# Performance work log

Hardware: AMD Instinct MI355X
Metric: run time of the kernel (lower is better)

## Reference

```python
import jax, jax.numpy as jnp
import numpy as np

EPS = 1e-5  # torch nn.LayerNorm default

def _ln(x, g, b):
    # LayerNorm over last dim with per-position affine params g, b (broadcastable)
    m = jnp.mean(x, axis=-1, keepdims=True)
    v = jnp.mean((x - m) ** 2, axis=-1, keepdims=True)
    return (x - m) * jax.lax.rsqrt(v + EPS) * g + b

def _mlp_ln(s, W1, b1, W2, b2, g, b):
    # Linear -> SiLU -> Linear -> LayerNorm
    h = jax.nn.silu(s @ W1 + b1) @ W2 + b2
    return _ln(h, g, b)

def setup_inputs() -> dict:
    key = jax.random.key(0)
    B, S, D = 4, 2048, 1024
    MEM, NOI, RES = 512, 64, 32
    ks = jax.random.split(key, 40)
    ki = iter(range(40))
    def nrm(shape, scale=0.02):
        return (jax.random.normal(ks[next(ki)], shape, jnp.float32) * scale)
    def gamma(shape):
        return jnp.ones(shape, jnp.float32) + nrm(shape)
    inp = {
        'x': jax.random.normal(ks[next(ki)], (B, S, D), jnp.float32),
        'pathway_ids': jax.random.randint(ks[next(ki)], (B, S), 0, 1000),
        'compartment_ids': jax.random.randint(ks[next(ki)], (B, S), 0, 5),
        'time_steps': jax.random.randint(ks[next(ki)], (B, S), 0, 5),
        'scale_type': jax.random.randint(ks[next(ki)], (B, S), 0, 3),
        'memory_state': jax.random.normal(ks[next(ki)], (B, MEM), jnp.float32),
        'noise_state': jax.random.normal(ks[next(ki)], (B, NOI), jnp.float32),
        'resource_state': jax.random.normal(ks[next(ki)], (B, RES), jnp.float32),
        # per-pathway / compartment / time / scale LayerNorm affine tables
        'pw_g': gamma((1000, D)), 'pw_b': nrm((1000, D)),
        'cp_g': gamma((5, D)), 'cp_b': nrm((5, D)),
        'tm_g': gamma((5, D)), 'tm_b': nrm((5, D)),
        'ms_g': gamma((3, D)), 'ms_b': nrm((3, D)),
        # memory / stochastic / resource MLP+LN stacks
        'mem_W1': nrm((MEM, D)), 'mem_b1': jnp.zeros((D,)), 'mem_W2': nrm((D, D)), 'mem_b2': jnp.zeros((D,)), 'mem_g': gamma((D,)), 'mem_be': jnp.zeros((D,)),
        'noi_W1': nrm((NOI, D)), 'noi_b1': jnp.zeros((D,)), 'noi_W2': nrm((D, D)), 'noi_b2': jnp.zeros((D,)), 'noi_g': gamma((D,)), 'noi_be': jnp.zeros((D,)),
        'res_W1': nrm((RES, D)), 'res_b1': jnp.zeros((D,)), 'res_W2': nrm((D, D)), 'res_b2': jnp.zeros((D,)), 'res_g': gamma((D,)), 'res_be': jnp.zeros((D,)),
        # integration MLP+LN
        'int_W1': nrm((6 * D, D)), 'int_b1': jnp.zeros((D,)), 'int_W2': nrm((D, D)), 'int_b2': jnp.zeros((D,)), 'int_g': gamma((D,)), 'int_be': jnp.zeros((D,)),
        'aw': jnp.ones((6,), jnp.float32) / 6.0,
    }
    return inp

def reference(x, pathway_ids, compartment_ids, time_steps, scale_type,
              memory_state, noise_state, resource_state,
              pw_g, pw_b, cp_g, cp_b, tm_g, tm_b, ms_g, ms_b,
              mem_W1, mem_b1, mem_W2, mem_b2, mem_g, mem_be,
              noi_W1, noi_b1, noi_W2, noi_b2, noi_g, noi_be,
              res_W1, res_b1, res_W2, res_b2, res_g, res_be,
              int_W1, int_b1, int_W2, int_b2, int_g, int_be, aw):
    # hierarchical: pathway-indexed LN, then compartment-indexed LN on its output
    h = _ln(x, pw_g[pathway_ids], pw_b[pathway_ids])
    h = _ln(h, cp_g[compartment_ids], cp_b[compartment_ids])
    # temporal: time-step-indexed LN of x
    t = _ln(x, tm_g[time_steps], tm_b[time_steps])
    # state-conditioned additive effects, broadcast over seq
    m = x + _mlp_ln(memory_state, mem_W1, mem_b1, mem_W2, mem_b2, mem_g, mem_be)[:, None, :]
    n = x + _mlp_ln(noise_state, noi_W1, noi_b1, noi_W2, noi_b2, noi_g, noi_be)[:, None, :]
    r = x + _mlp_ln(resource_state, res_W1, res_b1, res_W2, res_b2, res_g, res_be)[:, None, :]
    # multiscale: scale-indexed LN (scale in {0,1,2})
    s = _ln(x, ms_g[scale_type], ms_b[scale_type])
    w = jax.nn.softmax(aw)
    cat = jnp.concatenate([w[0] * h, w[1] * t, w[2] * m, w[3] * n, w[4] * r, w[5] * s], axis=-1)
    return _mlp_ln(cat, int_W1, int_b1, int_W2, int_b2, int_g, int_be)
```

## Files before the change

kernel.cpp:

```cpp
#include <hip/hip_runtime.h>
#include <cstdint>
#include <cstddef>

#define EPS_LN 1e-5f

typedef short bf16x8 __attribute__((ext_vector_type(8)));
typedef float f32x4 __attribute__((ext_vector_type(4)));
typedef unsigned int u32_gl __attribute__((address_space(1)));
typedef unsigned int u32_ld __attribute__((address_space(3)));

__device__ __forceinline__ unsigned short f2bf(float f) {
  union { float f; unsigned u; } v; v.f = f;
  unsigned r = v.u + 0x7fffu + ((v.u >> 16) & 1u);
  return (unsigned short)(r >> 16);
}

__device__ __forceinline__ float block_sum256(float v, float* red) {
  for (int m = 32; m > 0; m >>= 1) v += __shfl_xor(v, m, 64);
  const int lane = threadIdx.x & 63, w = threadIdx.x >> 6;
  if (lane == 0) red[w] = v;
  __syncthreads();
  float r = red[0] + red[1] + red[2] + red[3];
  __syncthreads();
  return r;
}

__global__ __launch_bounds__(256) void setup_small(
    const float* __restrict__ aw,
    const float* __restrict__ mb1, const float* __restrict__ nb1, const float* __restrict__ rb1,
    const float* __restrict__ mb2, const float* __restrict__ nb2, const float* __restrict__ rb2,
    const float* __restrict__ ib1,
    float* __restrict__ w, float* __restrict__ H1pre, float* __restrict__ Ys,
    float* __restrict__ bias1) {
  const int bi = blockIdx.x;
  if (bi == 0) {
    if (threadIdx.x == 0) {
      float m = aw[0];
      for (int i = 1; i < 6; ++i) m = fmaxf(m, aw[i]);
      float e[6], s = 0.f;
      for (int i = 0; i < 6; ++i) { e[i] = __expf(aw[i] - m); s += e[i]; }
      for (int i = 0; i < 6; ++i) w[i] = e[i] / s;
    }
    return;
  }
  if (bi <= 48) {
    const int idx = (bi - 1) * 256 + threadIdx.x;
    const int st = idx >> 12;
    const float* b1 = st == 0 ? mb1 : st == 1 ? nb1 : rb1;
    H1pre[idx] = b1[idx & 1023];
    return;
  }
  if (bi <= 96) {
    const int idx = (bi - 49) * 256 + threadIdx.x;
    const int st = idx >> 12;
    const float* b2 = st == 0 ? mb2 : st == 1 ? nb2 : rb2;
    Ys[idx] = b2[idx & 1023];
    return;
  }
  const int idx = (bi - 97) * 256 + threadIdx.x;
  bias1[idx] = ib1[idx & 1023];
}

__global__ __launch_bounds__(256) void state_h1_acc(
    const float* __restrict__ mem, const float* __restrict__ noi, const float* __restrict__ res,
    const float* __restrict__ mW1, const float* __restrict__ nW1, const float* __restrict__ rW1,
    float* __restrict__ H1pre) {
  const int chunk = blockIdx.x, ks = blockIdx.y;
  const int j = chunk * 128 + (threadIdx.x & 127);
  const int half = threadIdx.x >> 7;
  int st, k0, klen, sstride;
  const float* W1; const float* sp;
  if (ks < 8)       { st = 0; W1 = mW1; sp = mem; sstride = 512; k0 = ks * 64 + half * 32; klen = 32; }
  else if (ks == 8) { st = 1; W1 = nW1; sp = noi; sstride = 64;  k0 = half * 32;           klen = 32; }
  else              { st = 2; W1 = rW1; sp = res; sstride = 32;  k0 = half * 16;           klen = 16; }
  float a0 = 0.f, a1 = 0.f, a2 = 0.f, a3 = 0.f;
  const float* wp = W1 + (size_t)k0 * 1024 + j;
  for (int it = 0; it < klen; ++it) {
    const float wv = wp[(size_t)it * 1024];
    const int k = k0 + it;
    a0 += sp[k] * wv;
    a1 += sp[sstride + k] * wv;
    a2 += sp[2 * sstride + k] * wv;
    a3 += sp[3 * sstride + k] * wv;
  }
  __shared__ float part[4][128];
  const int jl = threadIdx.x & 127;
  if (half) { part[0][jl] = a0; part[1][jl] = a1; part[2][jl] = a2; part[3][jl] = a3; }
  __syncthreads();
  if (!half) {
    atomicAdd(&H1pre[(size_t)(st * 4 + 0) * 1024 + j], a0 + part[0][jl]);
    atomicAdd(&H1pre[(size_t)(st * 4 + 1) * 1024 + j], a1 + part[1][jl]);
    atomicAdd(&H1pre[(size_t)(st * 4 + 2) * 1024 + j], a2 + part[2][jl]);
    atomicAdd(&H1pre[(size_t)(st * 4 + 3) * 1024 + j], a3 + part[3][jl]);
  }
}

__global__ __launch_bounds__(256) void state_y_acc(
    const float* __restrict__ H1pre,
    const float* __restrict__ mW2, const float* __restrict__ nW2, const float* __restrict__ rW2,
    float* __restrict__ Ys) {
  const int chunk = blockIdx.x, ks = blockIdx.y, st = blockIdx.z;
  const float* W2 = st == 0 ? mW2 : st == 1 ? nW2 : rW2;
  const int j = chunk * 128 + (threadIdx.x & 127);
  const int half = threadIdx.x >> 7;
  const int k0 = ks * 64 + half * 32;
  const float* h1 = H1pre + (size_t)st * 4096;
  float a0 = 0.f, a1 = 0.f, a2 = 0.f, a3 = 0.f;
  const float* wp = W2 + (size_t)k0 * 1024 + j;
  for (int it = 0; it < 32; ++it) {
    const float wv = wp[(size_t)it * 1024];
    const int k = k0 + it;
    float h;
    h = h1[k];        a0 += (h / (1.f + __expf(-h))) * wv;
    h = h1[1024 + k]; a1 += (h / (1.f + __expf(-h))) * wv;
    h = h1[2048 + k]; a2 += (h / (1.f + __expf(-h))) * wv;
    h = h1[3072 + k]; a3 += (h / (1.f + __expf(-h))) * wv;
  }
  __shared__ float part[4][128];
  const int jl = threadIdx.x & 127;
  if (half) { part[0][jl] = a0; part[1][jl] = a1; part[2][jl] = a2; part[3][jl] = a3; }
  __syncthreads();
  if (!half) {
    atomicAdd(&Ys[(size_t)(st * 4 + 0) * 1024 + j], a0 + part[0][jl]);
    atomicAdd(&Ys[(size_t)(st * 4 + 1) * 1024 + j], a1 + part[1][jl]);
    atomicAdd(&Ys[(size_t)(st * 4 + 2) * 1024 + j], a2 + part[2][jl]);
    atomicAdd(&Ys[(size_t)(st * 4 + 3) * 1024 + j], a3 + part[3][jl]);
  }
}

__global__ __launch_bounds__(256) void state_ln(
    const float* __restrict__ Ys,
    const float* __restrict__ mg, const float* __restrict__ mbe,
    const float* __restrict__ ng, const float* __restrict__ nbe,
    const float* __restrict__ rg, const float* __restrict__ rbe,
    const float* __restrict__ w, float* __restrict__ mnrv) {
  __shared__ float red[4];
  const int st = blockIdx.x >> 2, b = blockIdx.x & 3;
  const float* g  = st == 0 ? mg  : st == 1 ? ng  : rg;
  const float* be = st == 0 ? mbe : st == 1 ? nbe : rbe;
  const float* y = Ys + (size_t)blockIdx.x * 1024;
  const int j = threadIdx.x * 4;
  float4 yv4 = *(const float4*)(y + j);
  float yv[4] = { yv4.x, yv4.y, yv4.z, yv4.w };
  float s = yv[0] + yv[1] + yv[2] + yv[3];
  float ss = yv[0]*yv[0] + yv[1]*yv[1] + yv[2]*yv[2] + yv[3]*yv[3];
  s = block_sum256(s, red);
  ss = block_sum256(ss, red);
  const float mu = s * (1.f / 1024.f);
  const float rstd = rsqrtf(ss * (1.f / 1024.f) - mu * mu + EPS_LN);
  float4 g4 = *(const float4*)(g + j);
  float4 b4 = *(const float4*)(be + j);
  const float sc = w[2 + st];
  float* out = mnrv + (size_t)b * 3072 + st * 1024;
  out[j]     = ((yv[0] - mu) * rstd * g4.x + b4.x) * sc;
  out[j + 1] = ((yv[1] - mu) * rstd * g4.y + b4.y) * sc;
  out[j + 2] = ((yv[2] - mu) * rstd * g4.z + b4.z) * sc;
  out[j + 3] = ((yv[3] - mu) * rstd * g4.w + b4.w) * sc;
}

__global__ __launch_bounds__(256) void bias1_kernel(
    const float* __restrict__ mnrv, const float* __restrict__ iW1,
    float* __restrict__ bias1) {
  const int chunk = blockIdx.x, ks = blockIdx.y;
  const int j = chunk * 128 + (threadIdx.x & 127);
  const int half = threadIdx.x >> 7;
  const int g0 = ks * 64 + half * 32;
  float acc0 = 0.f, acc1 = 0.f, acc2 = 0.f, acc3 = 0.f;
  const float* wp = iW1 + (size_t)(2048 + g0) * 1024 + j;
  for (int it = 0; it < 32; ++it) {
    const int g = g0 + it;
    const float wv = wp[(size_t)it * 1024];
    acc0 += mnrv[g] * wv;
    acc1 += mnrv[3072 + g] * wv;
    acc2 += mnrv[6144 + g] * wv;
    acc3 += mnrv[9216 + g] * wv;
  }
  __shared__ float part[4][128];
  const int jl = threadIdx.x & 127;
  if (half) { part[0][jl] = acc0; part[1][jl] = acc1; part[2][jl] = acc2; part[3][jl] = acc3; }
  __syncthreads();
  if (!half) {
    atomicAdd(&bias1[j],        acc0 + part[0][jl]);
    atomicAdd(&bias1[1024 + j], acc1 + part[1][jl]);
    atomicAdd(&bias1[2048 + j], acc2 + part[2][jl]);
    atomicAdd(&bias1[3072 + j], acc3 + part[3][jl]);
  }
}

__global__ __launch_bounds__(256) void build_w1t(
    const float* __restrict__ W1, const float* __restrict__ w,
    unsigned short* __restrict__ W1T) {
  __shared__ float tile[32][33];
  const int k0 = blockIdx.x * 32, n0 = blockIdx.y * 32;
  const int r = threadIdx.x >> 3;
  const int c = (threadIdx.x & 7) * 4;
  const int kk = k0 + r;
  float v[4];
  if (kk < 2048) {
    const float s = (kk < 1024) ? w[0] : w[1];
    float4 a = *(const float4*)(W1 + (size_t)kk * 1024 + n0 + c);
    v[0] = s * a.x; v[1] = s * a.y; v[2] = s * a.z; v[3] = s * a.w;
  } else if (kk < 3072) {
    const float s2 = w[2], s3 = w[3], s4 = w[4];
    float4 a = *(const float4*)(W1 + (size_t)kk * 1024 + n0 + c);
    float4 bq = *(const float4*)(W1 + (size_t)(kk + 1024) * 1024 + n0 + c);
    float4 cq = *(const float4*)(W1 + (size_t)(kk + 2048) * 1024 + n0 + c);
    v[0] = s2 * a.x + s3 * bq.x + s4 * cq.x;
    v[1] = s2 * a.y + s3 * bq.y + s4 * cq.y;
    v[2] = s2 * a.z + s3 * bq.z + s4 * cq.z;
    v[3] = s2 * a.w + s3 * bq.w + s4 * cq.w;
  } else {
    const float s = w[5];
    float4 a = *(const float4*)(W1 + (size_t)(kk + 2048) * 1024 + n0 + c);
    v[0] = s * a.x; v[1] = s * a.y; v[2] = s * a.z; v[3] = s * a.w;
  }
  tile[r][c] = v[0]; tile[r][c + 1] = v[1]; tile[r][c + 2] = v[2]; tile[r][c + 3] = v[3];
  __syncthreads();
  const int nl = threadIdx.x >> 3;
  const int k4 = (threadIdx.x & 7) * 4;
  ushort4 o;
  o.x = f2bf(tile[k4][nl]);     o.y = f2bf(tile[k4 + 1][nl]);
  o.z = f2bf(tile[k4 + 2][nl]); o.w = f2bf(tile[k4 + 3][nl]);
  *(ushort4*)(W1T + (size_t)(n0 + nl) * 4096 + k0 + k4) = o;
}

__global__ __launch_bounds__(256) void build_w2t(
    const float* __restrict__ W2, unsigned short* __restrict__ W2T) {
  __shared__ float tile[32][33];
  const int k0 = blockIdx.x * 32, n0 = blockIdx.y * 32;
  const int r = threadIdx.x >> 3, c = (threadIdx.x & 7) * 4;
  float4 a = *(const float4*)(W2 + (size_t)(k0 + r) * 1024 + n0 + c);
  tile[r][c] = a.x; tile[r][c + 1] = a.y; tile[r][c + 2] = a.z; tile[r][c + 3] = a.w;
  __syncthreads();
  const int nl = threadIdx.x >> 3, k4 = (threadIdx.x & 7) * 4;
  ushort4 o;
  o.x = f2bf(tile[k4][nl]);     o.y = f2bf(tile[k4 + 1][nl]);
  o.z = f2bf(tile[k4 + 2][nl]); o.w = f2bf(tile[k4 + 3][nl]);
  *(ushort4*)(W2T + (size_t)(n0 + nl) * 1024 + k0 + k4) = o;
}

__global__ __launch_bounds__(256) void build_cat(
    const float* __restrict__ x,
    const int* __restrict__ pid_, const int* __restrict__ cid_,
    const int* __restrict__ tid_, const int* __restrict__ sid_,
    const float* __restrict__ pwg, const float* __restrict__ pwb,
    const float* __restrict__ cpg, const float* __restrict__ cpb,
    const float* __restrict__ tmg, const float* __restrict__ tmb,
    const float* __restrict__ msg, const float* __restrict__ msb,
    unsigned short* __restrict__ cat4) {
  __shared__ float red[4];
  const int row = blockIdx.x;
  const int j = threadIdx.x * 4;
  float4 xv4 = *(const float4*)(x + (size_t)row * 1024 + j);
  float xv[4] = { xv4.x, xv4.y, xv4.z, xv4.w };
  float s = xv[0] + xv[1] + xv[2] + xv[3];
  float ss = xv[0]*xv[0] + xv[1]*xv[1] + xv[2]*xv[2] + xv[3]*xv[3];
  s = block_sum256(s, red);
  ss = block_sum256(ss, red);
  const float mu = s * (1.f / 1024.f);
  const float rstd = rsqrtf(ss * (1.f / 1024.f) - mu * mu + EPS_LN);
  float xh[4];
  for (int q = 0; q < 4; ++q) xh[q] = (xv[q] - mu) * rstd;
  const int pid = pid_[row], cid = cid_[row], tmi = tid_[row], msi = sid_[row];
  unsigned short* crow = cat4 + (size_t)row * 4096;

  float4 g4 = *(const float4*)(pwg + (size_t)pid * 1024 + j);
  float4 b4 = *(const float4*)(pwb + (size_t)pid * 1024 + j);
  float h1[4];
  h1[0] = xh[0] * g4.x + b4.x; h1[1] = xh[1] * g4.y + b4.y;
  h1[2] = xh[2] * g4.z + b4.z; h1[3] = xh[3] * g4.w + b4.w;
  float s1 = h1[0] + h1[1] + h1[2] + h1[3];
  float ss1 = h1[0]*h1[0] + h1[1]*h1[1] + h1[2]*h1[2] + h1[3]*h1[3];
  s1 = block_sum256(s1, red);
  ss1 = block_sum256(ss1, red);
  const float mu1 = s1 * (1.f / 1024.f);
  const float rstd1 = rsqrtf(ss1 * (1.f / 1024.f) - mu1 * mu1 + EPS_LN);
  g4 = *(const float4*)(cpg + (size_t)cid * 1024 + j);
  b4 = *(const float4*)(cpb + (size_t)cid * 1024 + j);
  ushort4 o;
  o.x = f2bf((h1[0] - mu1) * rstd1 * g4.x + b4.x);
  o.y = f2bf((h1[1] - mu1) * rstd1 * g4.y + b4.y);
  o.z = f2bf((h1[2] - mu1) * rstd1 * g4.z + b4.z);
  o.w = f2bf((h1[3] - mu1) * rstd1 * g4.w + b4.w);
  *(ushort4*)(crow + j) = o;

  g4 = *(const float4*)(tmg + (size_t)tmi * 1024 + j);
  b4 = *(const float4*)(tmb + (size_t)tmi * 1024 + j);
  o.x = f2bf(xh[0] * g4.x + b4.x); o.y = f2bf(xh[1] * g4.y + b4.y);
  o.z = f2bf(xh[2] * g4.z + b4.z); o.w = f2bf(xh[3] * g4.w + b4.w);
  *(ushort4*)(crow + 1024 + j) = o;

  o.x = f2bf(xv[0]); o.y = f2bf(xv[1]); o.z = f2bf(xv[2]); o.w = f2bf(xv[3]);
  *(ushort4*)(crow + 2048 + j) = o;

  g4 = *(const float4*)(msg + (size_t)msi * 1024 + j);
  b4 = *(const float4*)(msb + (size_t)msi * 1024 + j);
  o.x = f2bf(xh[0] * g4.x + b4.x); o.y = f2bf(xh[1] * g4.y + b4.y);
  o.z = f2bf(xh[2] * g4.z + b4.z); o.w = f2bf(xh[3] * g4.w + b4.w);
  *(ushort4*)(crow + 3072 + j) = o;
}

template <int EPI>
__global__ __launch_bounds__(128, 4) void gemm_bt(
    const unsigned short* __restrict__ A, const unsigned short* __restrict__ BT,
    const float* __restrict__ bias, void* __restrict__ out, int K) {
  __shared__ unsigned short At[64 * 32];
  __shared__ unsigned short Bt[128 * 32];
  const int t = threadIdx.x;
  const int lane = t & 63;
  const int wc = t >> 6;
  const int quad = lane >> 4, l16 = lane & 15;
  const int bm = blockIdx.x, bn = blockIdx.y;
  const unsigned short* Ab = A + (size_t)bm * 64 * K;
  const unsigned short* Bb = BT + (size_t)bn * 128 * K;
  const int r0 = t >> 2, c0 = (t & 3) * 8;
  f32x4 acc[4][4];
#pragma unroll
  for (int i = 0; i < 4; ++i)
#pragma unroll
    for (int jj = 0; jj < 4; ++jj) { f32x4 z = {0.f, 0.f, 0.f, 0.f}; acc[i][jj] = z; }

  for (int kt = 0; kt < K; kt += 32) {
    __builtin_amdgcn_global_load_lds(
        (const u32_gl*)(Ab + (size_t)r0 * K + kt + c0),
        (u32_ld*)(At + t * 8), 16, 0, 0);
    __builtin_amdgcn_global_load_lds(
        (const u32_gl*)(Ab + (size_t)(r0 + 32) * K + kt + c0),
        (u32_ld*)(At + (128 + t) * 8), 16, 0, 0);
    __builtin_amdgcn_global_load_lds(
        (const u32_gl*)(Bb + (size_t)r0 * K + kt + c0),
        (u32_ld*)(Bt + t * 8), 16, 0, 0);
    __builtin_amdgcn_global_load_lds(
        (const u32_gl*)(Bb + (size_t)(r0 + 32) * K + kt + c0),
        (u32_ld*)(Bt + (128 + t) * 8), 16, 0, 0);
    __builtin_amdgcn_global_load_lds(
        (const u32_gl*)(Bb + (size_t)(r0 + 64) * K + kt + c0),
        (u32_ld*)(Bt + (256 + t) * 8), 16, 0, 0);
    __builtin_amdgcn_global_load_lds(
        (const u32_gl*)(Bb + (size_t)(r0 + 96) * K + kt + c0),
        (u32_ld*)(Bt + (384 + t) * 8), 16, 0, 0);
    __syncthreads();
    bf16x8 aF[4], bF[4];
#pragma unroll
    for (int mi = 0; mi < 4; ++mi)
      aF[mi] = *(const bf16x8*)(At + (mi * 16 + l16) * 32 + quad * 8);
#pragma unroll
    for (int ni = 0; ni < 4; ++ni)
      bF[ni] = *(const bf16x8*)(Bt + (wc * 64 + ni * 16 + l16) * 32 + quad * 8);
#pragma unroll
    for (int mi = 0; mi < 4; ++mi)
#pragma unroll
      for (int ni = 0; ni < 4; ++ni)
        acc[mi][ni] = __builtin_amdgcn_mfma_f32_16x16x32_bf16(aF[mi], bF[ni], acc[mi][ni], 0, 0, 0);
    __syncthreads();
  }
#pragma unroll
  for (int mi = 0; mi < 4; ++mi) {
#pragma unroll
    for (int ni = 0; ni < 4; ++ni) {
      const int col = bn * 128 + wc * 64 + ni * 16 + l16;
#pragma unroll
      for (int r = 0; r < 4; ++r) {
        const int row = bm * 64 + mi * 16 + quad * 4 + r;
        float v = acc[mi][ni][r];
        if (EPI == 1) {
          v += bias[(size_t)(row >> 11) * 1024 + col];
          v = v / (1.f + __expf(-v));
          ((unsigned short*)out)[(size_t)row * 1024 + col] = f2bf(v);
        } else {
          v += bias[col];
          ((float*)out)[(size_t)row * 1024 + col] = v;
        }
      }
    }
  }
}

__global__ __launch_bounds__(256) void final_ln(
    const float* __restrict__ Y, const float* __restrict__ g,
    const float* __restrict__ be, float* __restrict__ out) {
  __shared__ float red[4];
  const int row = blockIdx.x;
  const int j = threadIdx.x * 4;
  float4 yv4 = *(const float4*)(Y + (size_t)row * 1024 + j);
  float yv[4] = { yv4.x, yv4.y, yv4.z, yv4.w };
  float s = yv[0] + yv[1] + yv[2] + yv[3];
  float ss = yv[0]*yv[0] + yv[1]*yv[1] + yv[2]*yv[2] + yv[3]*yv[3];
  s = block_sum256(s, red);
  ss = block_sum256(ss, red);
  const float mu = s * (1.f / 1024.f);
  const float rstd = rsqrtf(ss * (1.f / 1024.f) - mu * mu + EPS_LN);
  float4 g4 = *(const float4*)(g + j);
  float4 b4 = *(const float4*)(be + j);
  float4 o;
  o.x = (yv[0] - mu) * rstd * g4.x + b4.x;
  o.y = (yv[1] - mu) * rstd * g4.y + b4.y;
  o.z = (yv[2] - mu) * rstd * g4.z + b4.z;
  o.w = (yv[3] - mu) * rstd * g4.w + b4.w;
  *(float4*)(out + (size_t)row * 1024 + j) = o;
}

extern "C" void kernel_launch(void* const* d_in, const int* in_sizes, int n_in,
                              void* d_out, int out_size, void* d_ws, size_t ws_size,
                              hipStream_t stream) {
  const float* x   = (const float*)d_in[0];
  const int*   pid = (const int*)d_in[1];
  const int*   cid = (const int*)d_in[2];
  const int*   tms = (const int*)d_in[3];
  const int*   sct = (const int*)d_in[4];
  const float* mem = (const float*)d_in[5];
  const float* noi = (const float*)d_in[6];
  const float* res = (const float*)d_in[7];
  const float* pwg = (const float*)d_in[8];
  const float* pwb = (const float*)d_in[9];
  const float* cpg = (const float*)d_in[10];
  const float* cpb = (const float*)d_in[11];
  const float* tmg = (const float*)d_in[12];
  const float* tmb = (const float*)d_in[13];
  const float* msg = (const float*)d_in[14];
  const float* msb = (const float*)d_in[15];
  const float* mW1 = (const float*)d_in[16]; const float* mb1 = (const float*)d_in[17];
  const float* mW2 = (const float*)d_in[18]; const float* mb2 = (const float*)d_in[19];
  const float* mg  = (const float*)d_in[20]; const float* mbe = (const float*)d_in[21];
  const float* nW1 = (const float*)d_in[22]; const float* nb1 = (const float*)d_in[23];
  const float* nW2 = (const float*)d_in[24]; const float* nb2 = (const float*)d_in[25];
  const float* ng  = (const float*)d_in[26]; const float* nbe = (const float*)d_in[27];
  const float* rW1 = (const float*)d_in[28]; const float* rb1 = (const float*)d_in[29];
  const float* rW2 = (const float*)d_in[30]; const float* rb2 = (const float*)d_in[31];
  const float* rg  = (const float*)d_in[32]; const float* rbe = (const float*)d_in[33];
  const float* iW1 = (const float*)d_in[34]; const float* ib1 = (const float*)d_in[35];
  const float* iW2 = (const float*)d_in[36]; const float* ib2 = (const float*)d_in[37];
  const float* ig  = (const float*)d_in[38]; const float* ibe = (const float*)d_in[39];
  const float* aw  = (const float*)d_in[40];

  char* ws = (char*)d_ws;
  float* w6    = (float*)ws;
  float* H1pre = w6 + 16;
  float* Ys    = H1pre + 12288;
  float* mnrv  = Ys + 12288;
  float* bias1 = mnrv + 12288;
  unsigned short* W1T  = (unsigned short*)(ws + (1ull << 20));
  unsigned short* W2T  = (unsigned short*)(ws + (9ull << 20));
  unsigned short* cat4 = (unsigned short*)(ws + (11ull << 20));
  unsigned short* Hb   = (unsigned short*)(ws + (75ull << 20));
  float* Ybuf          = (float*)cat4;

  setup_small<<<113, 256, 0, stream>>>(aw, mb1, nb1, rb1, mb2, nb2, rb2, ib1,
                                       w6, H1pre, Ys, bias1);
  state_h1_acc<<<dim3(8, 10), 256, 0, stream>>>(mem, noi, res, mW1, nW1, rW1, H1pre);
  state_y_acc<<<dim3(8, 16, 3), 256, 0, stream>>>(H1pre, mW2, nW2, rW2, Ys);
  state_ln<<<12, 256, 0, stream>>>(Ys, mg, mbe, ng, nbe, rg, rbe, w6, mnrv);
  bias1_kernel<<<dim3(8, 48), 256, 0, stream>>>(mnrv, iW1, bias1);
  build_w1t<<<dim3(128, 32), 256, 0, stream>>>(iW1, w6, W1T);
  build_w2t<<<dim3(32, 32), 256, 0, stream>>>(iW2, W2T);
  build_cat<<<8192, 256, 0, stream>>>(x, pid, cid, tms, sct,
                                      pwg, pwb, cpg, cpb, tmg, tmb, msg, msb, cat4);
  gemm_bt<1><<<dim3(128, 8), 128, 0, stream>>>(cat4, W1T, bias1, (void*)Hb, 4096);
  gemm_bt<2><<<dim3(128, 8), 128, 0, stream>>>(Hb, W2T, ib2, (void*)Ybuf, 1024);
  final_ln<<<8192, 256, 0, stream>>>(Ybuf, ig, ibe, (float*)d_out);
}
```

Baseline: 405.6 us.

## Enlarge GEMM tiles to 128x128 with 4 waves, merge prep kernels, fold biases into atomics

The bf16 MFMA GEMM goes from 64x128 tiles with 2 waves to 128x128 tiles with 4 waves (a 2x2 wave grid). Each iteration now stages a 64-wide K slice as two 32-wide LDS halves, so there are fewer barriers per unit of K and more operand reuse per block. The activation build, W1 transpose/fold and W2 transpose kernels are merged into one launch. The setup kernel is replaced by a memset, with biases added inside the split-K atomics and softmax recomputed per block. The bigger tiles halve the grid (512 blocks) and raise LDS and register use, so occupancy and load balance could drop.

```diff
diff --git a/kernel.cpp b/kernel.cpp
--- a/kernel.cpp
+++ b/kernel.cpp
@@ -13,6 +13,15 @@
   union { float f; unsigned u; } v; v.f = f;
   unsigned r = v.u + 0x7fffu + ((v.u >> 16) & 1u);
   return (unsigned short)(r >> 16);
+}
+
+__device__ __forceinline__ void softmax6(const float* __restrict__ aw, float* w) {
+  float m = aw[0];
+  for (int i = 1; i < 6; ++i) m = fmaxf(m, aw[i]);
+  float s = 0.f;
+  for (int i = 0; i < 6; ++i) { w[i] = __expf(aw[i] - m); s += w[i]; }
+  const float inv = 1.f / s;
+  for (int i = 0; i < 6; ++i) w[i] *= inv;
 }
 
 __device__ __forceinline__ float block_sum256(float v, float* red) {
@@ -25,54 +34,19 @@
   return r;
 }
 
-__global__ __launch_bounds__(256) void setup_small(
-    const float* __restrict__ aw,
-    const float* __restrict__ mb1, const float* __restrict__ nb1, const float* __restrict__ rb1,
-    const float* __restrict__ mb2, const float* __restrict__ nb2, const float* __restrict__ rb2,
-    const float* __restrict__ ib1,
-    float* __restrict__ w, float* __restrict__ H1pre, float* __restrict__ Ys,
-    float* __restrict__ bias1) {
-  const int bi = blockIdx.x;
-  if (bi == 0) {
-    if (threadIdx.x == 0) {
-      float m = aw[0];
-      for (int i = 1; i < 6; ++i) m = fmaxf(m, aw[i]);
-      float e[6], s = 0.f;
-      for (int i = 0; i < 6; ++i) { e[i] = __expf(aw[i] - m); s += e[i]; }
-      for (int i = 0; i < 6; ++i) w[i] = e[i] / s;
-    }
-    return;
-  }
-  if (bi <= 48) {
-    const int idx = (bi - 1) * 256 + threadIdx.x;
-    const int st = idx >> 12;
-    const float* b1 = st == 0 ? mb1 : st == 1 ? nb1 : rb1;
-    H1pre[idx] = b1[idx & 1023];
-    return;
-  }
-  if (bi <= 96) {
-    const int idx = (bi - 49) * 256 + threadIdx.x;
-    const int st = idx >> 12;
-    const float* b2 = st == 0 ? mb2 : st == 1 ? nb2 : rb2;
-    Ys[idx] = b2[idx & 1023];
-    return;
-  }
-  const int idx = (bi - 97) * 256 + threadIdx.x;
-  bias1[idx] = ib1[idx & 1023];
-}
-
 __global__ __launch_bounds__(256) void state_h1_acc(
     const float* __restrict__ mem, const float* __restrict__ noi, const float* __restrict__ res,
     const float* __restrict__ mW1, const float* __restrict__ nW1, const float* __restrict__ rW1,
+    const float* __restrict__ mb1, const float* __restrict__ nb1, const float* __restrict__ rb1,
     float* __restrict__ H1pre) {
   const int chunk = blockIdx.x, ks = blockIdx.y;
   const int j = chunk * 128 + (threadIdx.x & 127);
   const int half = threadIdx.x >> 7;
   int st, k0, klen, sstride;
-  const float* W1; const float* sp;
-  if (ks < 8)       { st = 0; W1 = mW1; sp = mem; sstride = 512; k0 = ks * 64 + half * 32; klen = 32; }
-  else if (ks == 8) { st = 1; W1 = nW1; sp = noi; sstride = 64;  k0 = half * 32;           klen = 32; }
-  else              { st = 2; W1 = rW1; sp = res; sstride = 32;  k0 = half * 16;           klen = 16; }
+  const float* W1; const float* sp; const float* b1;
+  if (ks < 8)       { st = 0; W1 = mW1; sp = mem; b1 = mb1; sstride = 512; k0 = ks * 64 + half * 32; klen = 32; }
+  else if (ks == 8) { st = 1; W1 = nW1; sp = noi; b1 = nb1; sstride = 64;  k0 = half * 32;           klen = 32; }
+  else              { st = 2; W1 = rW1; sp = res; b1 = rb1; sstride = 32;  k0 = half * 16;           klen = 16; }
   float a0 = 0.f, a1 = 0.f, a2 = 0.f, a3 = 0.f;
   const float* wp = W1 + (size_t)k0 * 1024 + j;
   for (int it = 0; it < klen; ++it) {
@@ -88,19 +62,22 @@
   if (half) { part[0][jl] = a0; part[1][jl] = a1; part[2][jl] = a2; part[3][jl] = a3; }
   __syncthreads();
   if (!half) {
-    atomicAdd(&H1pre[(size_t)(st * 4 + 0) * 1024 + j], a0 + part[0][jl]);
-    atomicAdd(&H1pre[(size_t)(st * 4 + 1) * 1024 + j], a1 + part[1][jl]);
-    atomicAdd(&H1pre[(size_t)(st * 4 + 2) * 1024 + j], a2 + part[2][jl]);
-    atomicAdd(&H1pre[(size_t)(st * 4 + 3) * 1024 + j], a3 + part[3][jl]);
+    const float bv = (ks == 0 || ks >= 8) ? b1[j] : 0.f;
+    atomicAdd(&H1pre[(size_t)(st * 4 + 0) * 1024 + j], a0 + part[0][jl] + bv);
+    atomicAdd(&H1pre[(size_t)(st * 4 + 1) * 1024 + j], a1 + part[1][jl] + bv);
+    atomicAdd(&H1pre[(size_t)(st * 4 + 2) * 1024 + j], a2 + part[2][jl] + bv);
+    atomicAdd(&H1pre[(size_t)(st * 4 + 3) * 1024 + j], a3 + part[3][jl] + bv);
   }
 }
 
 __global__ __launch_bounds__(256) void state_y_acc(
     const float* __restrict__ H1pre,
     const float* __restrict__ mW2, const float* __restrict__ nW2, const float* __restrict__ rW2,
+    const float* __restrict__ mb2, const float* __restrict__ nb2, const float* __restrict__ rb2,
     float* __restrict__ Ys) {
   const int chunk = blockIdx.x, ks = blockIdx.y, st = blockIdx.z;
   const float* W2 = st == 0 ? mW2 : st == 1 ? nW2 : rW2;
+  const float* b2 = st == 0 ? mb2 : st == 1 ? nb2 : rb2;
   const int j = chunk * 128 + (threadIdx.x & 127);
   const int half = threadIdx.x >> 7;
   const int k0 = ks * 64 + half * 32;
@@ -121,10 +98,11 @@
   if (half) { part[0][jl] = a0; part[1][jl] = a1; part[2][jl] = a2; part[3][jl] = a3; }
   __syncthreads();
   if (!half) {
-    atomicAdd(&Ys[(size_t)(st * 4 + 0) * 1024 + j], a0 + part[0][jl]);
-    atomicAdd(&Ys[(size_t)(st * 4 + 1) * 1024 + j], a1 + part[1][jl]);
-    atomicAdd(&Ys[(size_t)(st * 4 + 2) * 1024 + j], a2 + part[2][jl]);
-    atomicAdd(&Ys[(size_t)(st * 4 + 3) * 1024 + j], a3 + part[3][jl]);
+    const float bv = (ks == 0) ? b2[j] : 0.f;
+    atomicAdd(&Ys[(size_t)(st * 4 + 0) * 1024 + j], a0 + part[0][jl] + bv);
+    atomicAdd(&Ys[(size_t)(st * 4 + 1) * 1024 + j], a1 + part[1][jl] + bv);
+    atomicAdd(&Ys[(size_t)(st * 4 + 2) * 1024 + j], a2 + part[2][jl] + bv);
+    atomicAdd(&Ys[(size_t)(st * 4 + 3) * 1024 + j], a3 + part[3][jl] + bv);
   }
 }
 
@@ -133,7 +111,7 @@
     const float* __restrict__ mg, const float* __restrict__ mbe,
     const float* __restrict__ ng, const float* __restrict__ nbe,
     const float* __restrict__ rg, const float* __restrict__ rbe,
-    const float* __restrict__ w, float* __restrict__ mnrv) {
+    const float* __restrict__ aw, float* __restrict__ mnrv) {
   __shared__ float red[4];
   const int st = blockIdx.x >> 2, b = blockIdx.x & 3;
   const float* g  = st == 0 ? mg  : st == 1 ? ng  : rg;
@@ -150,6 +128,8 @@
   const float rstd = rsqrtf(ss * (1.f / 1024.f) - mu * mu + EPS_LN);
   float4 g4 = *(const float4*)(g + j);
   float4 b4 = *(const float4*)(be + j);
+  float w[6];
+  softmax6(aw, w);
   const float sc = w[2 + st];
   float* out = mnrv + (size_t)b * 3072 + st * 1024;
   out[j]     = ((yv[0] - mu) * rstd * g4.x + b4.x) * sc;
@@ -160,7 +140,7 @@
 
 __global__ __launch_bounds__(256) void bias1_kernel(
     const float* __restrict__ mnrv, const float* __restrict__ iW1,
-    float* __restrict__ bias1) {
+    const float* __restrict__ ib1, float* __restrict__ bias1) {
   const int chunk = blockIdx.x, ks = blockIdx.y;
   const int j = chunk * 128 + (threadIdx.x & 127);
   const int half = threadIdx.x >> 7;
@@ -180,66 +160,15 @@
   if (half) { part[0][jl] = acc0; part[1][jl] = acc1; part[2][jl] = acc2; part[3][jl] = acc3; }
   __syncthreads();
   if (!half) {
-    atomicAdd(&bias1[j],        acc0 + part[0][jl]);
-    atomicAdd(&bias1[1024 + j], acc1 + part[1][jl]);
-    atomicAdd(&bias1[2048 + j], acc2 + part[2][jl]);
-    atomicAdd(&bias1[3072 + j], acc3 + part[3][jl]);
-  }
-}
-
-__global__ __launch_bounds__(256) void build_w1t(
-    const float* __restrict__ W1, const float* __restrict__ w,
-    unsigned short* __restrict__ W1T) {
-  __shared__ float tile[32][33];
-  const int k0 = blockIdx.x * 32, n0 = blockIdx.y * 32;
-  const int r = threadIdx.x >> 3;
-  const int c = (threadIdx.x & 7) * 4;
-  const int kk = k0 + r;
-  float v[4];
-  if (kk < 2048) {
-    const float s = (kk < 1024) ? w[0] : w[1];
-    float4 a = *(const float4*)(W1 + (size_t)kk * 1024 + n0 + c);
-    v[0] = s * a.x; v[1] = s * a.y; v[2] = s * a.z; v[3] = s * a.w;
-  } else if (kk < 3072) {
-    const float s2 = w[2], s3 = w[3], s4 = w[4];
-    float4 a = *(const float4*)(W1 + (size_t)kk * 1024 + n0 + c);
-    float4 bq = *(const float4*)(W1 + (size_t)(kk + 1024) * 1024 + n0 + c);
-    float4 cq = *(const float4*)(W1 + (size_t)(kk + 2048) * 1024 + n0 + c);
-    v[0] = s2 * a.x + s3 * bq.x + s4 * cq.x;
-    v[1] = s2 * a.y + s3 * bq.y + s4 * cq.y;
-    v[2] = s2 * a.z + s3 * bq.z + s4 * cq.z;
-    v[3] = s2 * a.w + s3 * bq.w + s4 * cq.w;
-  } else {
-    const float s = w[5];
-    float4 a = *(const float4*)(W1 + (size_t)(kk + 2048) * 1024 + n0 + c);
-    v[0] = s * a.x; v[1] = s * a.y; v[2] = s * a.z; v[3] = s * a.w;
-  }
-  tile[r][c] = v[0]; tile[r][c + 1] = v[1]; tile[r][c + 2] = v[2]; tile[r][c + 3] = v[3];
-  __syncthreads();
-  const int nl = threadIdx.x >> 3;
-  const int k4 = (threadIdx.x & 7) * 4;
-  ushort4 o;
-  o.x = f2bf(tile[k4][nl]);     o.y = f2bf(tile[k4 + 1][nl]);
-  o.z = f2bf(tile[k4 + 2][nl]); o.w = f2bf(tile[k4 + 3][nl]);
-  *(ushort4*)(W1T + (size_t)(n0 + nl) * 4096 + k0 + k4) = o;
-}
-
-__global__ __launch_bounds__(256) void build_w2t(
-    const float* __restrict__ W2, unsigned short* __restrict__ W2T) {
-  __shared__ float tile[32][33];
-  const int k0 = blockIdx.x * 32, n0 = blockIdx.y * 32;
-  const int r = threadIdx.x >> 3, c = (threadIdx.x & 7) * 4;
-  float4 a = *(const float4*)(W2 + (size_t)(k0 + r) * 1024 + n0 + c);
-  tile[r][c] = a.x; tile[r][c + 1] = a.y; tile[r][c + 2] = a.z; tile[r][c + 3] = a.w;
-  __syncthreads();
-  const int nl = threadIdx.x >> 3, k4 = (threadIdx.x & 7) * 4;
-  ushort4 o;
-  o.x = f2bf(tile[k4][nl]);     o.y = f2bf(tile[k4 + 1][nl]);
-  o.z = f2bf(tile[k4 + 2][nl]); o.w = f2bf(tile[k4 + 3][nl]);
-  *(ushort4*)(W2T + (size_t)(n0 + nl) * 1024 + k0 + k4) = o;
-}
-
-__global__ __launch_bounds__(256) void build_cat(
+    const float bv = (ks == 0) ? ib1[j] : 0.f;
+    atomicAdd(&bias1[j],        acc0 + part[0][jl] + bv);
+    atomicAdd(&bias1[1024 + j], acc1 + part[1][jl] + bv);
+    atomicAdd(&bias1[2048 + j], acc2 + part[2][jl] + bv);
+    atomicAdd(&bias1[3072 + j], acc3 + part[3][jl] + bv);
+  }
+}
+
+__global__ __launch_bounds__(256) void prep_all(
     const float* __restrict__ x,
     const int* __restrict__ pid_, const int* __restrict__ cid_,
     const int* __restrict__ tid_, const int* __restrict__ sid_,
@@ -247,71 +176,129 @@
     const float* __restrict__ cpg, const float* __restrict__ cpb,
     const float* __restrict__ tmg, const float* __restrict__ tmb,
     const float* __restrict__ msg, const float* __restrict__ msb,
-    unsigned short* __restrict__ cat4) {
+    const float* __restrict__ iW1, const float* __restrict__ iW2,
+    const float* __restrict__ aw,
+    unsigned short* __restrict__ cat4,
+    unsigned short* __restrict__ W1T, unsigned short* __restrict__ W2T) {
   __shared__ float red[4];
-  const int row = blockIdx.x;
-  const int j = threadIdx.x * 4;
-  float4 xv4 = *(const float4*)(x + (size_t)row * 1024 + j);
-  float xv[4] = { xv4.x, xv4.y, xv4.z, xv4.w };
-  float s = xv[0] + xv[1] + xv[2] + xv[3];
-  float ss = xv[0]*xv[0] + xv[1]*xv[1] + xv[2]*xv[2] + xv[3]*xv[3];
-  s = block_sum256(s, red);
-  ss = block_sum256(ss, red);
-  const float mu = s * (1.f / 1024.f);
-  const float rstd = rsqrtf(ss * (1.f / 1024.f) - mu * mu + EPS_LN);
-  float xh[4];
-  for (int q = 0; q < 4; ++q) xh[q] = (xv[q] - mu) * rstd;
-  const int pid = pid_[row], cid = cid_[row], tmi = tid_[row], msi = sid_[row];
-  unsigned short* crow = cat4 + (size_t)row * 4096;
-
-  float4 g4 = *(const float4*)(pwg + (size_t)pid * 1024 + j);
-  float4 b4 = *(const float4*)(pwb + (size_t)pid * 1024 + j);
-  float h1[4];
-  h1[0] = xh[0] * g4.x + b4.x; h1[1] = xh[1] * g4.y + b4.y;
-  h1[2] = xh[2] * g4.z + b4.z; h1[3] = xh[3] * g4.w + b4.w;
-  float s1 = h1[0] + h1[1] + h1[2] + h1[3];
-  float ss1 = h1[0]*h1[0] + h1[1]*h1[1] + h1[2]*h1[2] + h1[3]*h1[3];
-  s1 = block_sum256(s1, red);
-  ss1 = block_sum256(ss1, red);
-  const float mu1 = s1 * (1.f / 1024.f);
-  const float rstd1 = rsqrtf(ss1 * (1.f / 1024.f) - mu1 * mu1 + EPS_LN);
-  g4 = *(const float4*)(cpg + (size_t)cid * 1024 + j);
-  b4 = *(const float4*)(cpb + (size_t)cid * 1024 + j);
-  ushort4 o;
-  o.x = f2bf((h1[0] - mu1) * rstd1 * g4.x + b4.x);
-  o.y = f2bf((h1[1] - mu1) * rstd1 * g4.y + b4.y);
-  o.z = f2bf((h1[2] - mu1) * rstd1 * g4.z + b4.z);
-  o.w = f2bf((h1[3] - mu1) * rstd1 * g4.w + b4.w);
-  *(ushort4*)(crow + j) = o;
-
-  g4 = *(const float4*)(tmg + (size_t)tmi * 1024 + j);
-  b4 = *(const float4*)(tmb + (size_t)tmi * 1024 + j);
-  o.x = f2bf(xh[0] * g4.x + b4.x); o.y = f2bf(xh[1] * g4.y + b4.y);
-  o.z = f2bf(xh[2] * g4.z + b4.z); o.w = f2bf(xh[3] * g4.w + b4.w);
-  *(ushort4*)(crow + 1024 + j) = o;
-
-  o.x = f2bf(xv[0]); o.y = f2bf(xv[1]); o.z = f2bf(xv[2]); o.w = f2bf(xv[3]);
-  *(ushort4*)(crow + 2048 + j) = o;
-
-  g4 = *(const float4*)(msg + (size_t)msi * 1024 + j);
-  b4 = *(const float4*)(msb + (size_t)msi * 1024 + j);
-  o.x = f2bf(xh[0] * g4.x + b4.x); o.y = f2bf(xh[1] * g4.y + b4.y);
-  o.z = f2bf(xh[2] * g4.z + b4.z); o.w = f2bf(xh[3] * g4.w + b4.w);
-  *(ushort4*)(crow + 3072 + j) = o;
+  __shared__ float tile[32][33];
+  int bi = blockIdx.x;
+  if (bi < 8192) {
+    const int row = bi;
+    const int j = threadIdx.x * 4;
+    float4 xv4 = *(const float4*)(x + (size_t)row * 1024 + j);
+    float xv[4] = { xv4.x, xv4.y, xv4.z, xv4.w };
+    float s = xv[0] + xv[1] + xv[2] + xv[3];
+    float ss = xv[0]*xv[0] + xv[1]*xv[1] + xv[2]*xv[2] + xv[3]*xv[3];
+    s = block_sum256(s, red);
+    ss = block_sum256(ss, red);
+    const float mu = s * (1.f / 1024.f);
+    const float rstd = rsqrtf(ss * (1.f / 1024.f) - mu * mu + EPS_LN);
+    float xh[4];
+    for (int q = 0; q < 4; ++q) xh[q] = (xv[q] - mu) * rstd;
+    const int pid = pid_[row], cid = cid_[row], tmi = tid_[row], msi = sid_[row];
+    unsigned short* crow = cat4 + (size_t)row * 4096;
+
+    float4 g4 = *(const float4*)(pwg + (size_t)pid * 1024 + j);
+    float4 b4 = *(const float4*)(pwb + (size_t)pid * 1024 + j);
+    float h1[4];
+    h1[0] = xh[0] * g4.x + b4.x; h1[1] = xh[1] * g4.y + b4.y;
+    h1[2] = xh[2] * g4.z + b4.z; h1[3] = xh[3] * g4.w + b4.w;
+    float s1 = h1[0] + h1[1] + h1[2] + h1[3];
+    float ss1 = h1[0]*h1[0] + h1[1]*h1[1] + h1[2]*h1[2] + h1[3]*h1[3];
+    s1 = block_sum256(s1, red);
+    ss1 = block_sum256(ss1, red);
+    const float mu1 = s1 * (1.f / 1024.f);
+    const float rstd1 = rsqrtf(ss1 * (1.f / 1024.f) - mu1 * mu1 + EPS_LN);
+    g4 = *(const float4*)(cpg + (size_t)cid * 1024 + j);
+    b4 = *(const float4*)(cpb + (size_t)cid * 1024 + j);
+    ushort4 o;
+    o.x = f2bf((h1[0] - mu1) * rstd1 * g4.x + b4.x);
+    o.y = f2bf((h1[1] - mu1) * rstd1 * g4.y + b4.y);
+    o.z = f2bf((h1[2] - mu1) * rstd1 * g4.z + b4.z);
+    o.w = f2bf((h1[3] - mu1) * rstd1 * g4.w + b4.w);
+    *(ushort4*)(crow + j) = o;
+
+    g4 = *(const float4*)(tmg + (size_t)tmi * 1024 + j);
+    b4 = *(const float4*)(tmb + (size_t)tmi * 1024 + j);
+    o.x = f2bf(xh[0] * g4.x + b4.x); o.y = f2bf(xh[1] * g4.y + b4.y);
+    o.z = f2bf(xh[2] * g4.z + b4.z); o.w = f2bf(xh[3] * g4.w + b4.w);
+    *(ushort4*)(crow + 1024 + j) = o;
+
+    o.x = f2bf(xv[0]); o.y = f2bf(xv[1]); o.z = f2bf(xv[2]); o.w = f2bf(xv[3]);
+    *(ushort4*)(crow + 2048 + j) = o;
+
+    g4 = *(const float4*)(msg + (size_t)msi * 1024 + j);
+    b4 = *(const float4*)(msb + (size_t)msi * 1024 + j);
+    o.x = f2bf(xh[0] * g4.x + b4.x); o.y = f2bf(xh[1] * g4.y + b4.y);
+    o.z = f2bf(xh[2] * g4.z + b4.z); o.w = f2bf(xh[3] * g4.w + b4.w);
+    *(ushort4*)(crow + 3072 + j) = o;
+    return;
+  }
+  bi -= 8192;
+  float w[6];
+  softmax6(aw, w);
+  const int r = threadIdx.x >> 3;
+  const int c = (threadIdx.x & 7) * 4;
+  if (bi < 4096) {
+    const int k0 = (bi & 127) * 32, n0 = (bi >> 7) * 32;
+    const int kk = k0 + r;
+    float v[4];
+    if (kk < 2048) {
+      const float s = (kk < 1024) ? w[0] : w[1];
+      float4 a = *(const float4*)(iW1 + (size_t)kk * 1024 + n0 + c);
+      v[0] = s * a.x; v[1] = s * a.y; v[2] = s * a.z; v[3] = s * a.w;
+    } else if (kk < 3072) {
+      const float s2 = w[2], s3 = w[3], s4 = w[4];
+      float4 a = *(const float4*)(iW1 + (size_t)kk * 1024 + n0 + c);
+      float4 bq = *(const float4*)(iW1 + (size_t)(kk + 1024) * 1024 + n0 + c);
+      float4 cq = *(const float4*)(iW1 + (size_t)(kk + 2048) * 1024 + n0 + c);
+      v[0] = s2 * a.x + s3 * bq.x + s4 * cq.x;
+      v[1] = s2 * a.y + s3 * bq.y + s4 * cq.y;
+      v[2] = s2 * a.z + s3 * bq.z + s4 * cq.z;
+      v[3] = s2 * a.w + s3 * bq.w + s4 * cq.w;
+    } else {
+      const float s = w[5];
+      float4 a = *(const float4*)(iW1 + (size_t)(kk + 2048) * 1024 + n0 + c);
+      v[0] = s * a.x; v[1] = s * a.y; v[2] = s * a.z; v[3] = s * a.w;
+    }
+    tile[r][c] = v[0]; tile[r][c + 1] = v[1]; tile[r][c + 2] = v[2]; tile[r][c + 3] = v[3];
+    __syncthreads();
+    const int nl = threadIdx.x >> 3;
+    const int k4 = (threadIdx.x & 7) * 4;
+    ushort4 o;
+    o.x = f2bf(tile[k4][nl]);     o.y = f2bf(tile[k4 + 1][nl]);
+    o.z = f2bf(tile[k4 + 2][nl]); o.w = f2bf(tile[k4 + 3][nl]);
+    *(ushort4*)(W1T + (size_t)(n0 + nl) * 4096 + k0 + k4) = o;
+    return;
+  }
+  bi -= 4096;
+  {
+    const int k0 = (bi & 31) * 32, n0 = (bi >> 5) * 32;
+    float4 a = *(const float4*)(iW2 + (size_t)(k0 + r) * 1024 + n0 + c);
+    tile[r][c] = a.x; tile[r][c + 1] = a.y; tile[r][c + 2] = a.z; tile[r][c + 3] = a.w;
+    __syncthreads();
+    const int nl = threadIdx.x >> 3, k4 = (threadIdx.x & 7) * 4;
+    ushort4 o;
+    o.x = f2bf(tile[k4][nl]);     o.y = f2bf(tile[k4 + 1][nl]);
+    o.z = f2bf(tile[k4 + 2][nl]); o.w = f2bf(tile[k4 + 3][nl]);
+    *(ushort4*)(W2T + (size_t)(n0 + nl) * 1024 + k0 + k4) = o;
+  }
 }
 
 template <int EPI>
-__global__ __launch_bounds__(128, 4) void gemm_bt(
+__global__ __launch_bounds__(256, 2) void gemm_bt(
     const unsigned short* __restrict__ A, const unsigned short* __restrict__ BT,
     const float* __restrict__ bias, void* __restrict__ out, int K) {
-  __shared__ unsigned short At[64 * 32];
-  __shared__ unsigned short Bt[128 * 32];
+  __shared__ unsigned short At[2][128 * 32];
+  __shared__ unsigned short Bt[2][128 * 32];
   const int t = threadIdx.x;
   const int lane = t & 63;
-  const int wc = t >> 6;
+  const int wave = t >> 6;
+  const int wr = wave >> 1, wc = wave & 1;
   const int quad = lane >> 4, l16 = lane & 15;
   const int bm = blockIdx.x, bn = blockIdx.y;
-  const unsigned short* Ab = A + (size_t)bm * 64 * K;
+  const unsigned short* Ab = A + (size_t)bm * 128 * K;
   const unsigned short* Bb = BT + (size_t)bn * 128 * K;
   const int r0 = t >> 2, c0 = (t & 3) * 8;
   f32x4 acc[4][4];
@@ -320,38 +307,39 @@
 #pragma unroll
     for (int jj = 0; jj < 4; ++jj) { f32x4 z = {0.f, 0.f, 0.f, 0.f}; acc[i][jj] = z; }
 
-  for (int kt = 0; kt < K; kt += 32) {
-    __builtin_amdgcn_global_load_lds(
-        (const u32_gl*)(Ab + (size_t)r0 * K + kt + c0),
-        (u32_ld*)(At + t * 8), 16, 0, 0);
-    __builtin_amdgcn_global_load_lds(
-        (const u32_gl*)(Ab + (size_t)(r0 + 32) * K + kt + c0),
-        (u32_ld*)(At + (128 + t) * 8), 16, 0, 0);
-    __builtin_amdgcn_global_load_lds(
-        (const u32_gl*)(Bb + (size_t)r0 * K + kt + c0),
-        (u32_ld*)(Bt + t * 8), 16, 0, 0);
-    __builtin_amdgcn_global_load_lds(
-        (const u32_gl*)(Bb + (size_t)(r0 + 32) * K + kt + c0),
-        (u32_ld*)(Bt + (128 + t) * 8), 16, 0, 0);
-    __builtin_amdgcn_global_load_lds(
-        (const u32_gl*)(Bb + (size_t)(r0 + 64) * K + kt + c0),
-        (u32_ld*)(Bt + (256 + t) * 8), 16, 0, 0);
-    __builtin_amdgcn_global_load_lds(
-        (const u32_gl*)(Bb + (size_t)(r0 + 96) * K + kt + c0),
-        (u32_ld*)(Bt + (384 + t) * 8), 16, 0, 0);
+  for (int kt = 0; kt < K; kt += 64) {
+#pragma unroll
+    for (int h = 0; h < 2; ++h) {
+      const int ko = kt + h * 32;
+      __builtin_amdgcn_global_load_lds(
+          (const u32_gl*)(Ab + (size_t)r0 * K + ko + c0),
+          (u32_ld*)(At[h] + t * 8), 16, 0, 0);
+      __builtin_amdgcn_global_load_lds(
+          (const u32_gl*)(Ab + (size_t)(r0 + 64) * K + ko + c0),
+          (u32_ld*)(At[h] + (256 + t) * 8), 16, 0, 0);
+      __builtin_amdgcn_global_load_lds(
+          (const u32_gl*)(Bb + (size_t)r0 * K + ko + c0),
+          (u32_ld*)(Bt[h] + t * 8), 16, 0, 0);
+      __builtin_amdgcn_global_load_lds(
+          (const u32_gl*)(Bb + (size_t)(r0 + 64) * K + ko + c0),
+          (u32_ld*)(Bt[h] + (256 + t) * 8), 16, 0, 0);
+    }
     __syncthreads();
-    bf16x8 aF[4], bF[4];
-#pragma unroll
-    for (int mi = 0; mi < 4; ++mi)
-      aF[mi] = *(const bf16x8*)(At + (mi * 16 + l16) * 32 + quad * 8);
-#pragma unroll
-    for (int ni = 0; ni < 4; ++ni)
-      bF[ni] = *(const bf16x8*)(Bt + (wc * 64 + ni * 16 + l16) * 32 + quad * 8);
-#pragma unroll
-    for (int mi = 0; mi < 4; ++mi)
+#pragma unroll
+    for (int h = 0; h < 2; ++h) {
+      bf16x8 aF[4], bF[4];
+#pragma unroll
+      for (int mi = 0; mi < 4; ++mi)
+        aF[mi] = *(const bf16x8*)(At[h] + (wr * 64 + mi * 16 + l16) * 32 + quad * 8);
 #pragma unroll
       for (int ni = 0; ni < 4; ++ni)
-        acc[mi][ni] = __builtin_amdgcn_mfma_f32_16x16x32_bf16(aF[mi], bF[ni], acc[mi][ni], 0, 0, 0);
+        bF[ni] = *(const bf16x8*)(Bt[h] + (wc * 64 + ni * 16 + l16) * 32 + quad * 8);
+#pragma unroll
+      for (int mi = 0; mi < 4; ++mi)
+#pragma unroll
+        for (int ni = 0; ni < 4; ++ni)
+          acc[mi][ni] = __builtin_amdgcn_mfma_f32_16x16x32_bf16(aF[mi], bF[ni], acc[mi][ni], 0, 0, 0);
+    }
     __syncthreads();
   }
 #pragma unroll
@@ -361,7 +349,7 @@
       const int col = bn * 128 + wc * 64 + ni * 16 + l16;
 #pragma unroll
       for (int r = 0; r < 4; ++r) {
-        const int row = bm * 64 + mi * 16 + quad * 4 + r;
+        const int row = bm * 128 + wr * 64 + mi * 16 + quad * 4 + r;
         float v = acc[mi][ni][r];
         if (EPI == 1) {
           v += bias[(size_t)(row >> 11) * 1024 + col];
@@ -434,28 +422,27 @@
   const float* aw  = (const float*)d_in[40];
 
   char* ws = (char*)d_ws;
-  float* w6    = (float*)ws;
-  float* H1pre = w6 + 16;
+  float* H1pre = (float*)ws;
   float* Ys    = H1pre + 12288;
-  float* mnrv  = Ys + 12288;
-  float* bias1 = mnrv + 12288;
+  float* bias1 = Ys + 12288;
+  float* mnrv  = bias1 + 4096;
   unsigned short* W1T  = (unsigned short*)(ws + (1ull << 20));
   unsigned short* W2T  = (unsigned short*)(ws + (9ull << 20));
   unsigned short* cat4 = (unsigned short*)(ws + (11ull << 20));
   unsigned short* Hb   = (unsigned short*)(ws + (75ull << 20));
   float* Ybuf          = (float*)cat4;
 
-  setup_small<<<113, 256, 0, stream>>>(aw, mb1, nb1, rb1, mb2, nb2, rb2, ib1,
-                                       w6, H1pre, Ys, bias1);
-  state_h1_acc<<<dim3(8, 10), 256, 0, stream>>>(mem, noi, res, mW1, nW1, rW1, H1pre);
-  state_y_acc<<<dim3(8, 16, 3), 256, 0, stream>>>(H1pre, mW2, nW2, rW2, Ys);
-  state_ln<<<12, 256, 0, stream>>>(Ys, mg, mbe, ng, nbe, rg, rbe, w6, mnrv);
-  bias1_kernel<<<dim3(8, 48), 256, 0, stream>>>(mnrv, iW1, bias1);
-  build_w1t<<<dim3(128, 32), 256, 0, stream>>>(iW1, w6, W1T);
-  build_w2t<<<dim3(32, 32), 256, 0, stream>>>(iW2, W2T);
-  build_cat<<<8192, 256, 0, stream>>>(x, pid, cid, tms, sct,
-                                      pwg, pwb, cpg, cpb, tmg, tmb, msg, msb, cat4);
-  gemm_bt<1><<<dim3(128, 8), 128, 0, stream>>>(cat4, W1T, bias1, (void*)Hb, 4096);
-  gemm_bt<2><<<dim3(128, 8), 128, 0, stream>>>(Hb, W2T, ib2, (void*)Ybuf, 1024);
+  hipMemsetAsync(ws, 0, (12288 + 12288 + 4096) * sizeof(float), stream);
+  state_h1_acc<<<dim3(8, 10), 256, 0, stream>>>(mem, noi, res, mW1, nW1, rW1,
+                                                mb1, nb1, rb1, H1pre);
+  state_y_acc<<<dim3(8, 16, 3), 256, 0, stream>>>(H1pre, mW2, nW2, rW2,
+                                                  mb2, nb2, rb2, Ys);
+  state_ln<<<12, 256, 0, stream>>>(Ys, mg, mbe, ng, nbe, rg, rbe, aw, mnrv);
+  bias1_kernel<<<dim3(8, 48), 256, 0, stream>>>(mnrv, iW1, ib1, bias1);
+  prep_all<<<8192 + 4096 + 1024, 256, 0, stream>>>(
+      x, pid, cid, tms, sct, pwg, pwb, cpg, cpb, tmg, tmb, msg, msb,
+      iW1, iW2, aw, cat4, W1T, W2T);
+  gemm_bt<1><<<dim3(64, 8), 256, 0, stream>>>(cat4, W1T, bias1, (void*)Hb, 4096);
+  gemm_bt<2><<<dim3(64, 8), 256, 0, stream>>>(Hb, W2T, ib2, (void*)Ybuf, 1024);
   final_ln<<<8192, 256, 0, stream>>>(Ybuf, ig, ibe, (float*)d_out);
 }
```

New measurement: 371.5 us. -8.4%, faster.
